# Performance work log

Measured on AMD Instinct MI355X. Metric: run time of the kernel, lower is better.

Reference implementation:

```python
import jax, jax.numpy as jnp
import numpy as np

B, T, E, WIN, OC, VOCAB = 256, 2048, 128, 5, 128, 50000


def setup_inputs() -> dict:
    key = jax.random.key(0)
    k1, k2, k3, k4, k5, k6 = jax.random.split(key, 6)
    return {
        "x": jax.random.randint(k1, (B, T), 0, VOCAB + 1, dtype=jnp.int32),
        "emb_table": jax.random.normal(k2, (VOCAB + 1, E), dtype=jnp.float32),
        "att_w": jax.random.normal(k3, (WIN, E), dtype=jnp.float32) * 0.05,
        "att_b": jax.random.normal(k4, (1,), dtype=jnp.float32),
        "cnn_w": jax.random.normal(k5, (OC, E), dtype=jnp.float32) * 0.05,
        "cnn_b": jax.random.normal(k6, (OC,), dtype=jnp.float32),
    }


def reference(x, emb_table, att_w, att_b, cnn_w, cnn_b):
    win = att_w.shape[0]
    pad = (win - 1) // 2
    embed = emb_table[x]                                   # [B, T, E]
    x_pad = jnp.pad(embed, ((0, 0), (pad, pad), (0, 0)))
    T_ = embed.shape[1]
    # Sliding-window dot product over full embed dim (the degenerate Conv2d)
    s = jnp.zeros(embed.shape[:2], dtype=embed.dtype)      # [B, T]
    for k in range(win):
        s = s + jnp.einsum('bte,e->bt', x_pad[:, k:k + T_, :], att_w[k])
    scores = jax.nn.sigmoid(s + att_b[0])                  # [B, T]
    gated = embed * scores[:, :, None]                     # [B, T, E]
    feat = jnp.tanh(jnp.einsum('bte,oe->bto', gated, cnn_w) + cnn_b)  # [B, T, OC]
    out = jnp.max(feat, axis=1)                            # [B, OC] (maxpool over seq)
    return out[:, :, None, None]                           # [B, OC, 1, 1]
```

## Files before the change

### kernel.cpp

```cpp
#include <hip/hip_runtime.h>
#include <hip/hip_bf16.h>
#include <math.h>

#define B_   256
#define T_   2048
#define E_   128
#define WIN_ 5
#define PAD_ 2
#define OC_  128
#define VOCAB1 50001
#define NT   8
#define TT   64
#define BTOK (NT * TT)
#define REAL_ROWS (TT + WIN_ - 1)
#define ROWS 80
#define ASTR 136

#define NTAB_CH (VOCAB1 * E_ / 8)

typedef __attribute__((ext_vector_type(8))) short short8;
typedef __attribute__((ext_vector_type(4))) float floatx4;

static __device__ __forceinline__ short f2bf(float f) {
    union { __hip_bfloat16 h; short s; } u;
    u.h = __float2bfloat16(f);
    return u.s;
}

__device__ __forceinline__ void atomicMaxFloat(float* addr, float v) {
    if (v >= 0.0f) atomicMax((int*)addr, __float_as_int(v));
    else           atomicMin((unsigned int*)addr, __float_as_uint(v));
}

__global__ void prep_full(const float* __restrict__ emb, const float* __restrict__ cnn_w,
                          const float* __restrict__ att_w,
                          short* __restrict__ tab, short* __restrict__ wsw,
                          short* __restrict__ wsatt) {
    int i = blockIdx.x * 256 + threadIdx.x;
    const float* src;
    short* dst;
    if (i < NTAB_CH) { src = emb; dst = tab; }
    else if ((i -= NTAB_CH) < OC_ * E_ / 8) { src = cnn_w; dst = wsw; }
    else if ((i -= OC_ * E_ / 8) < WIN_ * E_ / 8) { src = att_w; dst = wsatt; }
    else return;
    const float4* s = (const float4*)src + (size_t)i * 2;
    float4 a = s[0], b = s[1];
    short8 o = { f2bf(a.x), f2bf(a.y), f2bf(a.z), f2bf(a.w),
                 f2bf(b.x), f2bf(b.y), f2bf(b.z), f2bf(b.w) };
    *(short8*)(dst + (size_t)i * 8) = o;
}

__global__ void prep_small(const float* __restrict__ cnn_w, const float* __restrict__ att_w,
                           short* __restrict__ wsw, short* __restrict__ wsatt) {
    int i = blockIdx.x * 256 + threadIdx.x;
    if (i < OC_ * E_)  wsw[i]   = f2bf(cnn_w[i]);
    if (i < WIN_ * E_) wsatt[i] = f2bf(att_w[i]);
}

template <bool TAB_BF16>
__launch_bounds__(256, 4)
__global__ void local_attn_main(const int* __restrict__ x,
                                const short* __restrict__ tab,
                                const float* __restrict__ emb,
                                const float* __restrict__ att_b_p,
                                const short* __restrict__ wsw,
                                const short* __restrict__ wsatt,
                                const float* __restrict__ cnn_b,
                                float* __restrict__ out) {
    __shared__ short sh_a[ROWS * ASTR];
    __shared__ short sh_att[16 * ASTR];
    __shared__ float sh_r[ROWS * 8];
    __shared__ float sh_score[TT];
    __shared__ int   sh_idx[NT * ROWS];

    const int tid  = threadIdx.x;
    const int lane = tid & 63;
    const int w    = tid >> 6;
    const int b    = blockIdx.y;
    const int t0   = blockIdx.x * BTOK;
    const int l15  = lane & 15;
    const int quad = lane >> 4;
    const int rbase = tid >> 4;
    const int c     = tid & 15;

    for (int i = tid; i < NT * ROWS; i += 256) {
        int tile = i / ROWS, row = i - tile * ROWS;
        int t = t0 + tile * TT + row - PAD_;
        sh_idx[i] = (row < REAL_ROWS && t >= 0 && t < T_) ? x[b * T_ + t] : -1;
    }
    {
        int o = tid >> 4, cc = tid & 15;
        short8 v = (short8){0,0,0,0,0,0,0,0};
        if (o < WIN_) v = *(const short8*)(wsatt + o * E_ + cc * 8);
        *(short8*)(&sh_att[o * ASTR + cc * 8]) = v;
    }
    short8 Bf[2][4];
    #pragma unroll
    for (int j = 0; j < 2; j++)
        #pragma unroll
        for (int ks = 0; ks < 4; ks++)
            Bf[j][ks] = *(const short8*)(wsw + (size_t)(w * 32 + j * 16 + l15) * E_ + ks * 32 + quad * 8);
    __syncthreads();

    short8 g[5];
    #pragma unroll
    for (int k = 0; k < 5; k++) {
        int row = rbase + 16 * k;
        int idx = sh_idx[row];
        short8 v = (short8){0,0,0,0,0,0,0,0};
        if (idx >= 0) {
            if (TAB_BF16) v = *(const short8*)(tab + (size_t)idx * E_ + c * 8);
            else {
                const float4* p = (const float4*)(emb + (size_t)idx * E_ + c * 8);
                float4 p0 = p[0], p1 = p[1];
                v = (short8){ f2bf(p0.x), f2bf(p0.y), f2bf(p0.z), f2bf(p0.w),
                              f2bf(p1.x), f2bf(p1.y), f2bf(p1.z), f2bf(p1.w) };
            }
        }
        g[k] = v;
    }
    #pragma unroll
    for (int k = 0; k < 5; k++)
        *(short8*)(&sh_a[(rbase + 16 * k) * ASTR + c * 8]) = g[k];
    __syncthreads();

    const float attb = att_b_p[0];
    float mm[2] = { -INFINITY, -INFINITY };

    for (int it = 0; it < NT; it++) {
        if (it + 1 < NT) {
            const int* idxp = &sh_idx[(it + 1) * ROWS];
            #pragma unroll
            for (int k = 0; k < 5; k++) {
                int idx = idxp[rbase + 16 * k];
                short8 v = (short8){0,0,0,0,0,0,0,0};
                if (idx >= 0) {
                    if (TAB_BF16) v = *(const short8*)(tab + (size_t)idx * E_ + c * 8);
                    else {
                        const float4* p = (const float4*)(emb + (size_t)idx * E_ + c * 8);
                        float4 p0 = p[0], p1 = p[1];
                        v = (short8){ f2bf(p0.x), f2bf(p0.y), f2bf(p0.z), f2bf(p0.w),
                                      f2bf(p1.x), f2bf(p1.y), f2bf(p1.z), f2bf(p1.w) };
                    }
                }
                g[k] = v;
            }
        }

        for (int mt = w; mt < 5; mt += 4) {
            floatx4 acc = (floatx4){0.f, 0.f, 0.f, 0.f};
            #pragma unroll
            for (int ks = 0; ks < 4; ks++) {
                short8 a  = *(const short8*)(&sh_a[(mt * 16 + l15) * ASTR + ks * 32 + quad * 8]);
                short8 bs = *(const short8*)(&sh_att[l15 * ASTR + ks * 32 + quad * 8]);
                acc = __builtin_amdgcn_mfma_f32_16x16x32_bf16(a, bs, acc, 0, 0, 0);
            }
            if (l15 < 8) {
                #pragma unroll
                for (int r = 0; r < 4; r++)
                    sh_r[(mt * 16 + quad * 4 + r) * 8 + l15] = acc[r];
            }
        }
        __syncthreads();

        if (tid < TT) {
            float s = attb;
            #pragma unroll
            for (int k = 0; k < WIN_; k++) s += sh_r[(tid + k) * 8 + k];
            sh_score[tid] = 1.0f / (1.0f + __expf(-s));
        }

        floatx4 acc[4][2];
        #pragma unroll
        for (int i = 0; i < 4; i++)
            #pragma unroll
            for (int j = 0; j < 2; j++) acc[i][j] = (floatx4){0.f, 0.f, 0.f, 0.f};

        #pragma unroll
        for (int ks = 0; ks < 4; ks++) {
            int ko = ks * 32 + quad * 8;
            #pragma unroll
            for (int i = 0; i < 4; i++) {
                short8 ai = *(const short8*)(&sh_a[(PAD_ + i * 16 + l15) * ASTR + ko]);
                acc[i][0] = __builtin_amdgcn_mfma_f32_16x16x32_bf16(ai, Bf[0][ks], acc[i][0], 0, 0, 0);
                acc[i][1] = __builtin_amdgcn_mfma_f32_16x16x32_bf16(ai, Bf[1][ks], acc[i][1], 0, 0, 0);
            }
        }
        __syncthreads();

        #pragma unroll
        for (int i = 0; i < 4; i++) {
            #pragma unroll
            for (int r = 0; r < 4; r++) {
                float sc = sh_score[i * 16 + quad * 4 + r];
                mm[0] = fmaxf(mm[0], sc * acc[i][0][r]);
                mm[1] = fmaxf(mm[1], sc * acc[i][1][r]);
            }
        }

        if (it + 1 < NT) {
            #pragma unroll
            for (int k = 0; k < 5; k++)
                *(short8*)(&sh_a[(rbase + 16 * k) * ASTR + c * 8]) = g[k];
            __syncthreads();
        }
    }

    #pragma unroll
    for (int j = 0; j < 2; j++) {
        float m = mm[j];
        m = fmaxf(m, __shfl_xor(m, 16));
        m = fmaxf(m, __shfl_xor(m, 32));
        if (lane < 16) {
            int o = w * 32 + j * 16 + lane;
            atomicMaxFloat(&out[b * OC_ + o], tanhf(m + cnn_b[o]));
        }
    }
}

extern "C" void kernel_launch(void* const* d_in, const int* in_sizes, int n_in,
                              void* d_out, int out_size, void* d_ws, size_t ws_size,
                              hipStream_t stream) {
    const int*   x     = (const int*)d_in[0];
    const float* emb   = (const float*)d_in[1];
    const float* att_w = (const float*)d_in[2];
    const float* att_b = (const float*)d_in[3];
    const float* cnn_w = (const float*)d_in[4];
    const float* cnn_b = (const float*)d_in[5];
    float* out = (float*)d_out;

    hipMemsetAsync(d_out, 0xFF, (size_t)B_ * OC_ * sizeof(float), stream);

    const size_t tab_elems = (size_t)VOCAB1 * E_;
    const size_t need = tab_elems * 2 + OC_ * E_ * 2 + WIN_ * E_ * 2 + 64;

    dim3 grid(T_ / BTOK, B_);

    if (ws_size >= need) {
        short* tab    = (short*)d_ws;
        short* ws_w   = tab + tab_elems;
        short* ws_att = ws_w + OC_ * E_;
        int total = NTAB_CH + OC_ * E_ / 8 + WIN_ * E_ / 8;
        prep_full<<<(total + 255) / 256, 256, 0, stream>>>(emb, cnn_w, att_w, tab, ws_w, ws_att);
        local_attn_main<true><<<grid, 256, 0, stream>>>(x, tab, emb, att_b, ws_w, ws_att, cnn_b, out);
    } else {
        short* ws_w   = (short*)d_ws;
        short* ws_att = ws_w + OC_ * E_;
        prep_small<<<16, 256, 0, stream>>>(cnn_w, att_w, ws_w, ws_att);
        local_attn_main<false><<<grid, 256, 0, stream>>>(x, (const short*)nullptr, emb, att_b, ws_w, ws_att, cnn_b, out);
    }
}
```

Before: 123.8 us.

## Precompute per-vocab projection tables and gather them instead of per-token GEMM

Since the score is a scalar per token, gated@W^T equals score times (emb@W^T), so the projection is precomputed once per vocabulary row (50001x128 bf16) along with the per-window attention dot products. The main kernel then only gathers these table rows, computes sigmoid scores, and takes a scaled max, with no per-token MFMA. The table build runs on every call, so the cost moves from B*T GEMM work to a vocab-sized GEMM plus bf16 gathers. The fallback path is also reordered to issue the next tile's loads after the attention MFMA.

```diff
diff --git a/kernel.cpp b/kernel.cpp
--- a/kernel.cpp
+++ b/kernel.cpp
@@ -8,15 +8,13 @@
 #define WIN_ 5
 #define PAD_ 2
 #define OC_  128
+#define VOCAB_MAX 50000
 #define VOCAB1 50001
-#define NT   8
 #define TT   64
-#define BTOK (NT * TT)
 #define REAL_ROWS (TT + WIN_ - 1)
 #define ROWS 80
 #define ASTR 136
-
-#define NTAB_CH (VOCAB1 * E_ / 8)
+#define VROWS 64
 
 typedef __attribute__((ext_vector_type(8))) short short8;
 typedef __attribute__((ext_vector_type(4))) float floatx4;
@@ -32,22 +30,159 @@
     else           atomicMin((unsigned int*)addr, __float_as_uint(v));
 }
 
-__global__ void prep_full(const float* __restrict__ emb, const float* __restrict__ cnn_w,
-                          const float* __restrict__ att_w,
-                          short* __restrict__ tab, short* __restrict__ wsw,
-                          short* __restrict__ wsatt) {
-    int i = blockIdx.x * 256 + threadIdx.x;
-    const float* src;
-    short* dst;
-    if (i < NTAB_CH) { src = emb; dst = tab; }
-    else if ((i -= NTAB_CH) < OC_ * E_ / 8) { src = cnn_w; dst = wsw; }
-    else if ((i -= OC_ * E_ / 8) < WIN_ * E_ / 8) { src = att_w; dst = wsatt; }
-    else return;
-    const float4* s = (const float4*)src + (size_t)i * 2;
-    float4 a = s[0], b = s[1];
-    short8 o = { f2bf(a.x), f2bf(a.y), f2bf(a.z), f2bf(a.w),
-                 f2bf(b.x), f2bf(b.y), f2bf(b.z), f2bf(b.w) };
-    *(short8*)(dst + (size_t)i * 8) = o;
+__launch_bounds__(256, 2)
+__global__ void build_tables(const float* __restrict__ emb,
+                             const float* __restrict__ cnn_w,
+                             const float* __restrict__ att_w,
+                             short* __restrict__ D,
+                             float* __restrict__ r) {
+    __shared__ short sh_a[VROWS * ASTR];
+
+    const int tid  = threadIdx.x;
+    const int lane = tid & 63;
+    const int w    = tid >> 6;
+    const int l15  = lane & 15;
+    const int quad = lane >> 4;
+    const int v0   = blockIdx.x * VROWS;
+
+    #pragma unroll
+    for (int t = 0; t < 8; t++) {
+        int i   = t * 256 + tid;
+        int row = i >> 5, c4 = i & 31;
+        int vr  = v0 + row; if (vr > VOCAB_MAX) vr = VOCAB_MAX;
+        float4 v = *(const float4*)(emb + (size_t)vr * E_ + c4 * 4);
+        short4 o; o.x = f2bf(v.x); o.y = f2bf(v.y); o.z = f2bf(v.z); o.w = f2bf(v.w);
+        *(short4*)(&sh_a[row * ASTR + c4 * 4]) = o;
+    }
+
+    short8 Bf[2][4];
+    #pragma unroll
+    for (int j = 0; j < 2; j++)
+        #pragma unroll
+        for (int ks = 0; ks < 4; ks++) {
+            const float4* p = (const float4*)(cnn_w + (size_t)(w * 32 + j * 16 + l15) * E_ + ks * 32 + quad * 8);
+            float4 p0 = p[0], p1 = p[1];
+            Bf[j][ks] = (short8){ f2bf(p0.x), f2bf(p0.y), f2bf(p0.z), f2bf(p0.w),
+                                  f2bf(p1.x), f2bf(p1.y), f2bf(p1.z), f2bf(p1.w) };
+        }
+
+    short8 Ba[4];
+    #pragma unroll
+    for (int ks = 0; ks < 4; ks++) {
+        short8 v = (short8){0,0,0,0,0,0,0,0};
+        if (l15 < WIN_) {
+            const float4* p = (const float4*)(att_w + (size_t)l15 * E_ + ks * 32 + quad * 8);
+            float4 p0 = p[0], p1 = p[1];
+            v = (short8){ f2bf(p0.x), f2bf(p0.y), f2bf(p0.z), f2bf(p0.w),
+                          f2bf(p1.x), f2bf(p1.y), f2bf(p1.z), f2bf(p1.w) };
+        }
+        Ba[ks] = v;
+    }
+    __syncthreads();
+
+    #pragma unroll
+    for (int mt = 0; mt < 4; mt++) {
+        short8 a[4];
+        #pragma unroll
+        for (int ks = 0; ks < 4; ks++)
+            a[ks] = *(const short8*)(&sh_a[(mt * 16 + l15) * ASTR + ks * 32 + quad * 8]);
+        #pragma unroll
+        for (int j = 0; j < 2; j++) {
+            floatx4 acc = (floatx4){0.f, 0.f, 0.f, 0.f};
+            #pragma unroll
+            for (int ks = 0; ks < 4; ks++)
+                acc = __builtin_amdgcn_mfma_f32_16x16x32_bf16(a[ks], Bf[j][ks], acc, 0, 0, 0);
+            #pragma unroll
+            for (int rr = 0; rr < 4; rr++) {
+                int v = v0 + mt * 16 + quad * 4 + rr;
+                if (v <= VOCAB_MAX)
+                    D[(size_t)v * E_ + w * 32 + j * 16 + l15] = f2bf(acc[rr]);
+            }
+        }
+    }
+
+    {
+        short8 a[4];
+        #pragma unroll
+        for (int ks = 0; ks < 4; ks++)
+            a[ks] = *(const short8*)(&sh_a[(w * 16 + l15) * ASTR + ks * 32 + quad * 8]);
+        floatx4 acc = (floatx4){0.f, 0.f, 0.f, 0.f};
+        #pragma unroll
+        for (int ks = 0; ks < 4; ks++)
+            acc = __builtin_amdgcn_mfma_f32_16x16x32_bf16(a[ks], Ba[ks], acc, 0, 0, 0);
+        if (l15 < 8) {
+            #pragma unroll
+            for (int rr = 0; rr < 4; rr++) {
+                int v = v0 + w * 16 + quad * 4 + rr;
+                if (v <= VOCAB_MAX) r[(size_t)v * 8 + l15] = acc[rr];
+            }
+        }
+    }
+}
+
+__launch_bounds__(256, 8)
+__global__ void score_max(const int* __restrict__ x,
+                          const short* __restrict__ D,
+                          const float* __restrict__ r,
+                          const float* __restrict__ att_b_p,
+                          const float* __restrict__ cnn_b,
+                          float* __restrict__ out) {
+    __shared__ int   sh_x[260];
+    __shared__ float sh_sc[256];
+    __shared__ float sh_red[4][128];
+
+    const int tid  = threadIdx.x;
+    const int lane = tid & 63;
+    const int w    = tid >> 6;
+    const int b    = blockIdx.y;
+    const int t0   = blockIdx.x * 256;
+
+    for (int i = tid; i < 260; i += 256) {
+        int t = t0 + i - PAD_;
+        sh_x[i] = (t >= 0 && t < T_) ? x[b * T_ + t] : -1;
+    }
+    __syncthreads();
+
+    {
+        float s = att_b_p[0];
+        #pragma unroll
+        for (int k = 0; k < WIN_; k++) {
+            int v = sh_x[tid + k];
+            if (v >= 0) s += r[(size_t)v * 8 + k];
+        }
+        sh_sc[tid] = 1.0f / (1.0f + __expf(-s));
+    }
+    __syncthreads();
+
+    float mm0 = -INFINITY, mm1 = -INFINITY;
+    const int base_t = w * 64;
+    for (int i0 = 0; i0 < 64; i0 += 8) {
+        unsigned u[8];
+        float sc8[8];
+        #pragma unroll
+        for (int j = 0; j < 8; j++) {
+            int tok = base_t + i0 + j;
+            int v   = sh_x[tok + PAD_];
+            sc8[j]  = sh_sc[tok];
+            u[j]    = *(const unsigned*)(D + (size_t)v * E_ + lane * 2);
+        }
+        #pragma unroll
+        for (int j = 0; j < 8; j++) {
+            float lo = __uint_as_float(u[j] << 16);
+            float hi = __uint_as_float(u[j] & 0xFFFF0000u);
+            mm0 = fmaxf(mm0, sc8[j] * lo);
+            mm1 = fmaxf(mm1, sc8[j] * hi);
+        }
+    }
+
+    sh_red[w][lane * 2]     = mm0;
+    sh_red[w][lane * 2 + 1] = mm1;
+    __syncthreads();
+    if (tid < 128) {
+        float m = fmaxf(fmaxf(sh_red[0][tid], sh_red[1][tid]),
+                        fmaxf(sh_red[2][tid], sh_red[3][tid]));
+        atomicMaxFloat(&out[b * OC_ + tid], tanhf(m + cnn_b[tid]));
+    }
 }
 
 __global__ void prep_small(const float* __restrict__ cnn_w, const float* __restrict__ att_w,
@@ -57,33 +192,31 @@
     if (i < WIN_ * E_) wsatt[i] = f2bf(att_w[i]);
 }
 
-template <bool TAB_BF16>
 __launch_bounds__(256, 4)
-__global__ void local_attn_main(const int* __restrict__ x,
-                                const short* __restrict__ tab,
-                                const float* __restrict__ emb,
-                                const float* __restrict__ att_b_p,
-                                const short* __restrict__ wsw,
-                                const short* __restrict__ wsatt,
-                                const float* __restrict__ cnn_b,
-                                float* __restrict__ out) {
+__global__ void fallback_main(const int* __restrict__ x,
+                              const float* __restrict__ emb,
+                              const float* __restrict__ att_b_p,
+                              const short* __restrict__ wsw,
+                              const short* __restrict__ wsatt,
+                              const float* __restrict__ cnn_b,
+                              float* __restrict__ out) {
     __shared__ short sh_a[ROWS * ASTR];
     __shared__ short sh_att[16 * ASTR];
     __shared__ float sh_r[ROWS * 8];
     __shared__ float sh_score[TT];
-    __shared__ int   sh_idx[NT * ROWS];
+    __shared__ int   sh_idx[8 * ROWS];
 
     const int tid  = threadIdx.x;
     const int lane = tid & 63;
     const int w    = tid >> 6;
     const int b    = blockIdx.y;
-    const int t0   = blockIdx.x * BTOK;
+    const int t0   = blockIdx.x * (8 * TT);
     const int l15  = lane & 15;
     const int quad = lane >> 4;
     const int rbase = tid >> 4;
     const int c     = tid & 15;
 
-    for (int i = tid; i < NT * ROWS; i += 256) {
+    for (int i = tid; i < 8 * ROWS; i += 256) {
         int tile = i / ROWS, row = i - tile * ROWS;
         int t = t0 + tile * TT + row - PAD_;
         sh_idx[i] = (row < REAL_ROWS && t >= 0 && t < T_) ? x[b * T_ + t] : -1;
@@ -105,17 +238,13 @@
     short8 g[5];
     #pragma unroll
     for (int k = 0; k < 5; k++) {
-        int row = rbase + 16 * k;
-        int idx = sh_idx[row];
+        int idx = sh_idx[rbase + 16 * k];
         short8 v = (short8){0,0,0,0,0,0,0,0};
         if (idx >= 0) {
-            if (TAB_BF16) v = *(const short8*)(tab + (size_t)idx * E_ + c * 8);
-            else {
-                const float4* p = (const float4*)(emb + (size_t)idx * E_ + c * 8);
-                float4 p0 = p[0], p1 = p[1];
-                v = (short8){ f2bf(p0.x), f2bf(p0.y), f2bf(p0.z), f2bf(p0.w),
-                              f2bf(p1.x), f2bf(p1.y), f2bf(p1.z), f2bf(p1.w) };
-            }
+            const float4* p = (const float4*)(emb + (size_t)idx * E_ + c * 8);
+            float4 p0 = p[0], p1 = p[1];
+            v = (short8){ f2bf(p0.x), f2bf(p0.y), f2bf(p0.z), f2bf(p0.w),
+                          f2bf(p1.x), f2bf(p1.y), f2bf(p1.z), f2bf(p1.w) };
         }
         g[k] = v;
     }
@@ -127,42 +256,39 @@
     const float attb = att_b_p[0];
     float mm[2] = { -INFINITY, -INFINITY };
 
-    for (int it = 0; it < NT; it++) {
-        if (it + 1 < NT) {
+    for (int it = 0; it < 8; it++) {
+        for (int mt = w; mt < 5; mt += 4) {
+            floatx4 acc = (floatx4){0.f, 0.f, 0.f, 0.f};
+            #pragma unroll
+            for (int ks = 0; ks < 4; ks++) {
+                short8 a  = *(const short8*)(&sh_a[(mt * 16 + l15) * ASTR + ks * 32 + quad * 8]);
+                short8 bs = *(const short8*)(&sh_att[l15 * ASTR + ks * 32 + quad * 8]);
+                acc = __builtin_amdgcn_mfma_f32_16x16x32_bf16(a, bs, acc, 0, 0, 0);
+            }
+            if (l15 < 8) {
+                #pragma unroll
+                for (int r = 0; r < 4; r++)
+                    sh_r[(mt * 16 + quad * 4 + r) * 8 + l15] = acc[r];
+            }
+        }
+        __syncthreads();
+
+        if (it + 1 < 8) {
             const int* idxp = &sh_idx[(it + 1) * ROWS];
             #pragma unroll
             for (int k = 0; k < 5; k++) {
                 int idx = idxp[rbase + 16 * k];
                 short8 v = (short8){0,0,0,0,0,0,0,0};
                 if (idx >= 0) {
-                    if (TAB_BF16) v = *(const short8*)(tab + (size_t)idx * E_ + c * 8);
-                    else {
-                        const float4* p = (const float4*)(emb + (size_t)idx * E_ + c * 8);
-                        float4 p0 = p[0], p1 = p[1];
-                        v = (short8){ f2bf(p0.x), f2bf(p0.y), f2bf(p0.z), f2bf(p0.w),
-                                      f2bf(p1.x), f2bf(p1.y), f2bf(p1.z), f2bf(p1.w) };
-                    }
+                    const float4* p = (const float4*)(emb + (size_t)idx * E_ + c * 8);
+                    float4 p0 = p[0], p1 = p[1];
+                    v = (short8){ f2bf(p0.x), f2bf(p0.y), f2bf(p0.z), f2bf(p0.w),
+                                  f2bf(p1.x), f2bf(p1.y), f2bf(p1.z), f2bf(p1.w) };
                 }
                 g[k] = v;
             }
         }
 
-        for (int mt = w; mt < 5; mt += 4) {
-            floatx4 acc = (floatx4){0.f, 0.f, 0.f, 0.f};
-            #pragma unroll
-            for (int ks = 0; ks < 4; ks++) {
-                short8 a  = *(const short8*)(&sh_a[(mt * 16 + l15) * ASTR + ks * 32 + quad * 8]);
-                short8 bs = *(const short8*)(&sh_att[l15 * ASTR + ks * 32 + quad * 8]);
-                acc = __builtin_amdgcn_mfma_f32_16x16x32_bf16(a, bs, acc, 0, 0, 0);
-            }
-            if (l15 < 8) {
-                #pragma unroll
-                for (int r = 0; r < 4; r++)
-                    sh_r[(mt * 16 + quad * 4 + r) * 8 + l15] = acc[r];
-            }
-        }
-        __syncthreads();
-
         if (tid < TT) {
             float s = attb;
             #pragma unroll
@@ -175,7 +301,6 @@
         for (int i = 0; i < 4; i++)
             #pragma unroll
             for (int j = 0; j < 2; j++) acc[i][j] = (floatx4){0.f, 0.f, 0.f, 0.f};
-
         #pragma unroll
         for (int ks = 0; ks < 4; ks++) {
             int ko = ks * 32 + quad * 8;
@@ -198,7 +323,7 @@
             }
         }
 
-        if (it + 1 < NT) {
+        if (it + 1 < 8) {
             #pragma unroll
             for (int k = 0; k < 5; k++)
                 *(short8*)(&sh_a[(rbase + 16 * k) * ASTR + c * 8]) = g[k];
@@ -231,22 +356,21 @@
 
     hipMemsetAsync(d_out, 0xFF, (size_t)B_ * OC_ * sizeof(float), stream);
 
-    const size_t tab_elems = (size_t)VOCAB1 * E_;
-    const size_t need = tab_elems * 2 + OC_ * E_ * 2 + WIN_ * E_ * 2 + 64;
-
-    dim3 grid(T_ / BTOK, B_);
+    const size_t d_elems = (size_t)VOCAB1 * E_;
+    const size_t r_elems = (size_t)VOCAB1 * 8;
+    const size_t need = d_elems * 2 + r_elems * 4 + 64;
 
     if (ws_size >= need) {
-        short* tab    = (short*)d_ws;
-        short* ws_w   = tab + tab_elems;
-        short* ws_att = ws_w + OC_ * E_;
-        int total = NTAB_CH + OC_ * E_ / 8 + WIN_ * E_ / 8;
-        prep_full<<<(total + 255) / 256, 256, 0, stream>>>(emb, cnn_w, att_w, tab, ws_w, ws_att);
-        local_attn_main<true><<<grid, 256, 0, stream>>>(x, tab, emb, att_b, ws_w, ws_att, cnn_b, out);
+        short* Dt = (short*)d_ws;
+        float* rt = (float*)(Dt + d_elems);
+        build_tables<<<(VOCAB1 + VROWS - 1) / VROWS, 256, 0, stream>>>(emb, cnn_w, att_w, Dt, rt);
+        dim3 grid(T_ / 256, B_);
+        score_max<<<grid, 256, 0, stream>>>(x, Dt, rt, att_b, cnn_b, out);
     } else {
         short* ws_w   = (short*)d_ws;
         short* ws_att = ws_w + OC_ * E_;
         prep_small<<<16, 256, 0, stream>>>(cnn_w, att_w, ws_w, ws_att);
-        local_attn_main<false><<<grid, 256, 0, stream>>>(x, (const short*)nullptr, emb, att_b, ws_w, ws_att, cnn_b, out);
-    }
-}
+        dim3 grid(T_ / (8 * TT), B_);
+        fallback_main<<<grid, 256, 0, stream>>>(x, emb, att_b, ws_w, ws_att, cnn_b, out);
+    }
+}
```

Result: faster. 119.1 us (-3.8%).
